# Performance work log

Measured on AMD Instinct MI355X. Metric: run time of the kernel, lower is better.

The kernel has to match this reference:

```python
import jax, jax.numpy as jnp
import numpy as np

N, F, B = 4096, 2048, 2048


def setup_inputs() -> dict:
    key = jax.random.key(0)
    ks = jax.random.split(key, 11)
    s_h = 1.0 / np.sqrt(F).astype(np.float32)
    s_x = 1.0 / np.sqrt(B).astype(np.float32)
    inp = {
        "behavior": jax.random.normal(ks[0], (N, B), jnp.float32),
        "h0": jax.random.normal(ks[1], (N, F), jnp.float32),
        "c0": jax.random.normal(ks[2], (N, F), jnp.float32),
        "Wi_h": jax.random.normal(ks[3], (F, F), jnp.float32) * s_h,
        "Wi_x": jax.random.normal(ks[4], (B, F), jnp.float32) * s_x,
        "bi": jnp.zeros((F,), jnp.float32),
        "Wf_h": jax.random.normal(ks[5], (F, F), jnp.float32) * s_h,
        "Wf_x": jax.random.normal(ks[6], (B, F), jnp.float32) * s_x,
        "bf": jnp.zeros((F,), jnp.float32),
        "Wg_h": jax.random.normal(ks[7], (F, F), jnp.float32) * s_h,
        "Wg_x": jax.random.normal(ks[8], (B, F), jnp.float32) * s_x,
        "bg": jnp.zeros((F,), jnp.float32),
        "Wo_h": jax.random.normal(ks[9], (F, F), jnp.float32) * s_h,
        "Wo_x": jax.random.normal(ks[10], (B, F), jnp.float32) * s_x,
        "bo": jnp.zeros((F,), jnp.float32),
    }
    return inp


def reference(behavior, h0, c0, Wi_h, Wi_x, bi, Wf_h, Wf_x, bf,
              Wg_h, Wg_x, bg, Wo_h, Wo_x, bo):
    # Single-step LSTM cell: each gate is a two-input linear proj (h, behavior)
    def proj(Wh, Wx, b):
        return h0 @ Wh + behavior @ Wx + b  # [N, F]

    i = jax.nn.sigmoid(proj(Wi_h, Wi_x, bi))
    f = jax.nn.sigmoid(proj(Wf_h, Wf_x, bf))
    g = jnp.tanh(proj(Wg_h, Wg_x, bg))
    o = jax.nn.sigmoid(proj(Wo_h, Wo_x, bo))
    c = f * c0 + i * g
    h = o * jnp.tanh(c)
    return h
```

## Files before the change

kernel.cpp:

```cpp
#include <hip/hip_runtime.h>
#include <stdint.h>

#define N_ROWS 4096
#define F_DIM  2048
#define B_DIM  2048
#define K_DIM  4096

typedef __attribute__((ext_vector_type(8)))  __bf16 bf16x8;
typedef __attribute__((ext_vector_type(16))) float  f32x16;
typedef unsigned short u16;

__device__ __forceinline__ u16 f2bf(float x) {
  unsigned int u = __float_as_uint(x);
  u += 0x7fffu + ((u >> 16) & 1u);
  return (u16)(u >> 16);
}

__device__ __forceinline__ void async_copy16(const void* g, void* l) {
  __builtin_amdgcn_global_load_lds(
      (const __attribute__((address_space(1))) void*)g,
      (__attribute__((address_space(3))) void*)l, 16, 0, 0);
}

__device__ __forceinline__ float sigmoid_f(float x) {
  return 1.0f / (1.0f + __expf(-x));
}
__device__ __forceinline__ float tanh_f(float x) {
  float e2 = __expf(2.0f * x);
  return 1.0f - 2.0f / (e2 + 1.0f);
}

__device__ __forceinline__ f32x16 mm(bf16x8 a, bf16x8 b, f32x16 c) {
  return __builtin_amdgcn_mfma_f32_32x32x16_bf16(a, b, c, 0, 0, 0);
}

__global__ __launch_bounds__(256) void pack_x_kernel(
    const float* __restrict__ h0, const float* __restrict__ behavior,
    u16* __restrict__ Xc)
{
  int tid = blockIdx.x * 256 + threadIdx.x;
  int row = tid >> 9;
  int k0  = (tid & 511) * 8;
  const float* src = (k0 < F_DIM) ? (h0 + (size_t)row * F_DIM + k0)
                                  : (behavior + (size_t)row * B_DIM + (k0 - F_DIM));
  const float4* s4 = (const float4*)src;
  float4 a = s4[0], b = s4[1];
  uint4 o;
  o.x = (unsigned)f2bf(a.x) | ((unsigned)f2bf(a.y) << 16);
  o.y = (unsigned)f2bf(a.z) | ((unsigned)f2bf(a.w) << 16);
  o.z = (unsigned)f2bf(b.x) | ((unsigned)f2bf(b.y) << 16);
  o.w = (unsigned)f2bf(b.z) | ((unsigned)f2bf(b.w) << 16);
  *(uint4*)(Xc + (size_t)tid * 8) = o;
}

__global__ __launch_bounds__(256) void pack_w_kernel(
    const float* __restrict__ wi_h, const float* __restrict__ wi_x,
    const float* __restrict__ wf_h, const float* __restrict__ wf_x,
    const float* __restrict__ wg_h, const float* __restrict__ wg_x,
    const float* __restrict__ wo_h, const float* __restrict__ wo_x,
    u16* __restrict__ WT)
{
  __shared__ float tileT[32 * 65];
  int g = blockIdx.z;
  const float* Wh = (g == 0) ? wi_h : (g == 1) ? wf_h : (g == 2) ? wg_h : wo_h;
  const float* Wx = (g == 0) ? wi_x : (g == 1) ? wf_x : (g == 2) ? wg_x : wo_x;
  int fb = blockIdx.x * 32;
  int kb = blockIdx.y * 64;
  const float* W = (kb < F_DIM) ? Wh : Wx;
  int kofs = (kb < F_DIM) ? kb : (kb - F_DIM);

  int t  = threadIdx.x;
  int c4 = t & 7;
  int kr = t >> 3;
#pragma unroll
  for (int p = 0; p < 2; ++p) {
    int k_l = kr + p * 32;
    float4 v = *(const float4*)(W + (size_t)(kofs + k_l) * F_DIM + fb + c4 * 4);
    tileT[(c4 * 4 + 0) * 65 + k_l] = v.x;
    tileT[(c4 * 4 + 1) * 65 + k_l] = v.y;
    tileT[(c4 * 4 + 2) * 65 + k_l] = v.z;
    tileT[(c4 * 4 + 3) * 65 + k_l] = v.w;
  }
  __syncthreads();
  {
    int f_l = t >> 3;
    int k8  = (t & 7) * 8;
    const float* s = tileT + f_l * 65 + k8;
    uint4 o;
    o.x = (unsigned)f2bf(s[0]) | ((unsigned)f2bf(s[1]) << 16);
    o.y = (unsigned)f2bf(s[2]) | ((unsigned)f2bf(s[3]) << 16);
    o.z = (unsigned)f2bf(s[4]) | ((unsigned)f2bf(s[5]) << 16);
    o.w = (unsigned)f2bf(s[6]) | ((unsigned)f2bf(s[7]) << 16);
    *(uint4*)(WT + ((size_t)g * F_DIM + fb + f_l) * K_DIM + kb + k8) = o;
  }
}

__global__ __launch_bounds__(512, 2) void lstm_gemm_kernel(
    const u16* __restrict__ Xc, const u16* __restrict__ WT,
    const float* __restrict__ c0,
    const float* __restrict__ bi, const float* __restrict__ bff,
    const float* __restrict__ bg, const float* __restrict__ bo,
    float* __restrict__ out)
{
  __shared__ u16 Ls[32768];

  const int tid  = threadIdx.x;
  const int lane = tid & 63;
  const int wv   = tid >> 6;
  const int bm   = blockIdx.x;
  const int bn   = blockIdx.y;

  const int rw   = wv & 3;
  const int fh   = wv >> 2;
  const int l31  = lane & 31;
  const int half = lane >> 5;
  const int swb  = (l31 >> 1) & 3;

  const u16* aSrc[2];
  const u16* bSrc[2];
#pragma unroll
  for (int p = 0; p < 2; ++p) {
    int c = p * 512 + tid;
    int r = c >> 2, s = c & 3;
    int o = s ^ ((r >> 1) & 3);
    aSrc[p] = Xc + (size_t)(bm * 256 + r) * K_DIM + o * 8;
    int g = c >> 8, cc = c & 255;
    int rb = cc >> 2, sb2 = cc & 3;
    int ob = sb2 ^ ((rb >> 1) & 3);
    bSrc[p] = WT + ((size_t)g * F_DIM + bn * 64 + rb) * K_DIM + ob * 8;
  }
  const unsigned ub = (unsigned)(tid & ~63) * 16u;

  f32x16 acc[4][2];
#pragma unroll
  for (int g = 0; g < 4; ++g)
#pragma unroll
    for (int rh = 0; rh < 2; ++rh)
#pragma unroll
      for (int r = 0; r < 16; ++r) acc[g][rh][r] = 0.f;

#pragma unroll
  for (int p = 0; p < 2; ++p) {
    async_copy16(aSrc[p], (char*)Ls + p * 8192 + ub);
    async_copy16(bSrc[p], (char*)Ls + 16384 + p * 8192 + ub);
  }
#pragma unroll
  for (int p = 0; p < 2; ++p) { aSrc[p] += 32; bSrc[p] += 32; }

  int cur = 0;
  for (int kt = 0; kt < 128; ++kt) {
    const int nb = cur ^ 1;
    char* LdsN = (char*)Ls + nb * 32768;
    const u16* Lb = Ls + cur * 16384;
    const u16* Ab0 = Lb + (rw * 64 +      l31) * 32;
    const u16* Ab1 = Lb + (rw * 64 + 32 + l31) * 32;
    const u16* Bb  = Lb + 8192 + (fh * 32 + l31) * 32;

    if (kt < 127) {
      async_copy16(aSrc[0], LdsN + ub);
      async_copy16(bSrc[0], LdsN + 16384 + ub);
      asm volatile("s_waitcnt vmcnt(2)" ::: "memory");
    } else {
      asm volatile("s_waitcnt vmcnt(0)" ::: "memory");
    }
    __builtin_amdgcn_s_barrier();
    {
      const int sw8 = (half ^ swb) * 8;
      bf16x8 af0 = *(const bf16x8*)(Ab0 + sw8);
      bf16x8 af1 = *(const bf16x8*)(Ab1 + sw8);
      bf16x8 bfr[4];
#pragma unroll
      for (int g = 0; g < 4; ++g)
        bfr[g] = *(const bf16x8*)(Bb + g * 2048 + sw8);
      __builtin_amdgcn_s_setprio(1);
#pragma unroll
      for (int g = 0; g < 4; ++g) {
        acc[g][0] = mm(af0, bfr[g], acc[g][0]);
        acc[g][1] = mm(af1, bfr[g], acc[g][1]);
      }
      __builtin_amdgcn_s_setprio(0);
    }
    __builtin_amdgcn_s_barrier();

    {
      const int sw8 = ((2 + half) ^ swb) * 8;
      bf16x8 af0 = *(const bf16x8*)(Ab0 + sw8);
      bf16x8 af1 = *(const bf16x8*)(Ab1 + sw8);
      bf16x8 bfr[4];
#pragma unroll
      for (int g = 0; g < 4; ++g)
        bfr[g] = *(const bf16x8*)(Bb + g * 2048 + sw8);
      if (kt < 127) {
        async_copy16(aSrc[1], LdsN + 8192 + ub);
        async_copy16(bSrc[1], LdsN + 16384 + 8192 + ub);
      }
      __builtin_amdgcn_s_barrier();
      __builtin_amdgcn_s_setprio(1);
#pragma unroll
      for (int g = 0; g < 4; ++g) {
        acc[g][0] = mm(af0, bfr[g], acc[g][0]);
        acc[g][1] = mm(af1, bfr[g], acc[g][1]);
      }
      __builtin_amdgcn_s_setprio(0);
    }
    asm volatile("s_waitcnt lgkmcnt(0)" ::: "memory");
    __builtin_amdgcn_s_barrier();

#pragma unroll
    for (int p = 0; p < 2; ++p) { aSrc[p] += 32; bSrc[p] += 32; }
    cur ^= 1;
  }

  {
    int f = bn * 64 + fh * 32 + l31;
    float b0 = bi[f], b1 = bff[f], b2 = bg[f], b3 = bo[f];
#pragma unroll
    for (int rh = 0; rh < 2; ++rh) {
      int row_base = bm * 256 + rw * 64 + rh * 32 + 4 * half;
#pragma unroll
      for (int r = 0; r < 16; ++r) {
        int row = row_base + (r & 3) + 8 * (r >> 2);
        size_t idx = (size_t)row * F_DIM + f;
        float pi = acc[0][rh][r] + b0;
        float pf = acc[1][rh][r] + b1;
        float pg = acc[2][rh][r] + b2;
        float po = acc[3][rh][r] + b3;
        float iv = sigmoid_f(pi);
        float fv = sigmoid_f(pf);
        float gv = tanh_f(pg);
        float ov = sigmoid_f(po);
        float cv = fv * c0[idx] + iv * gv;
        out[idx] = ov * tanh_f(cv);
      }
    }
  }
}

extern "C" void kernel_launch(void* const* d_in, const int* in_sizes, int n_in,
                              void* d_out, int out_size, void* d_ws, size_t ws_size,
                              hipStream_t stream) {
  const float* behavior = (const float*)d_in[0];
  const float* h0       = (const float*)d_in[1];
  const float* c0       = (const float*)d_in[2];
  const float* Wi_h     = (const float*)d_in[3];
  const float* Wi_x     = (const float*)d_in[4];
  const float* bi       = (const float*)d_in[5];
  const float* Wf_h     = (const float*)d_in[6];
  const float* Wf_x     = (const float*)d_in[7];
  const float* bf       = (const float*)d_in[8];
  const float* Wg_h     = (const float*)d_in[9];
  const float* Wg_x     = (const float*)d_in[10];
  const float* bg       = (const float*)d_in[11];
  const float* Wo_h     = (const float*)d_in[12];
  const float* Wo_x     = (const float*)d_in[13];
  const float* bo       = (const float*)d_in[14];
  float* out = (float*)d_out;

  u16* Xc = (u16*)d_ws;
  u16* WT = Xc + (size_t)N_ROWS * K_DIM;

  pack_x_kernel<<<dim3(N_ROWS * (K_DIM / 8) / 256), 256, 0, stream>>>(h0, behavior, Xc);
  pack_w_kernel<<<dim3(F_DIM / 32, K_DIM / 64, 4), 256, 0, stream>>>(
      Wi_h, Wi_x, Wf_h, Wf_x, Wg_h, Wg_x, Wo_h, Wo_x, WT);
  lstm_gemm_kernel<<<dim3(N_ROWS / 256, F_DIM / 64), 512, 0, stream>>>(
      Xc, WT, c0, bi, bf, bg, bo, out);
}
```

Baseline: 536.0 us.

## Double K tile to 64 per stage with 8-wide XOR swizzle and fewer barriers

Each pipeline stage now covers 64 K elements instead of 32, so the loop runs 64 iterations with 8 async copies per thread per stage. The intermediate barriers and split prefetch of the old two-half structure are gone. The LDS swizzle changes from a 4-way to an 8-way XOR pattern to match the 128-byte row stride. LDS use doubles to 128 KB per block, which may hurt occupancy under the two-blocks-per-CU launch bound and will exceed the per-block LDS limit if it is 64 KB.

```diff
diff --git a/kernel.cpp b/kernel.cpp
--- a/kernel.cpp
+++ b/kernel.cpp
@@ -102,7 +102,7 @@
     const float* __restrict__ bg, const float* __restrict__ bo,
     float* __restrict__ out)
 {
-  __shared__ u16 Ls[32768];
+  __shared__ u16 Ls[2 * 32768];
 
   const int tid  = threadIdx.x;
   const int lane = tid & 63;
@@ -114,20 +114,23 @@
   const int fh   = wv >> 2;
   const int l31  = lane & 31;
   const int half = lane >> 5;
-  const int swb  = (l31 >> 1) & 3;
-
-  const u16* aSrc[2];
-  const u16* bSrc[2];
-#pragma unroll
-  for (int p = 0; p < 2; ++p) {
+  const int sA   = l31 & 7;
+
+  const u16* src[8];
+#pragma unroll
+  for (int p = 0; p < 8; ++p) {
     int c = p * 512 + tid;
-    int r = c >> 2, s = c & 3;
-    int o = s ^ ((r >> 1) & 3);
-    aSrc[p] = Xc + (size_t)(bm * 256 + r) * K_DIM + o * 8;
-    int g = c >> 8, cc = c & 255;
-    int rb = cc >> 2, sb2 = cc & 3;
-    int ob = sb2 ^ ((rb >> 1) & 3);
-    bSrc[p] = WT + ((size_t)g * F_DIM + bn * 64 + rb) * K_DIM + ob * 8;
+    if (p < 4) {
+      int r = c >> 3, s = c & 7;
+      int o = s ^ (r & 7);
+      src[p] = Xc + (size_t)(bm * 256 + r) * K_DIM + o * 8;
+    } else {
+      int cb = c - 2048;
+      int g = cb >> 9, cc = cb & 511;
+      int rb = cc >> 3, sb = cc & 7;
+      int ob = sb ^ (rb & 7);
+      src[p] = WT + ((size_t)g * F_DIM + bn * 64 + rb) * K_DIM + ob * 8;
+    }
   }
   const unsigned ub = (unsigned)(tid & ~63) * 16u;
 
@@ -140,38 +143,39 @@
       for (int r = 0; r < 16; ++r) acc[g][rh][r] = 0.f;
 
 #pragma unroll
-  for (int p = 0; p < 2; ++p) {
-    async_copy16(aSrc[p], (char*)Ls + p * 8192 + ub);
-    async_copy16(bSrc[p], (char*)Ls + 16384 + p * 8192 + ub);
-  }
-#pragma unroll
-  for (int p = 0; p < 2; ++p) { aSrc[p] += 32; bSrc[p] += 32; }
+  for (int p = 0; p < 8; ++p)
+    async_copy16(src[p], (char*)Ls + p * 8192 + ub);
+#pragma unroll
+  for (int p = 0; p < 8; ++p) src[p] += 64;
 
   int cur = 0;
-  for (int kt = 0; kt < 128; ++kt) {
-    const int nb = cur ^ 1;
-    char* LdsN = (char*)Ls + nb * 32768;
-    const u16* Lb = Ls + cur * 16384;
-    const u16* Ab0 = Lb + (rw * 64 +      l31) * 32;
-    const u16* Ab1 = Lb + (rw * 64 + 32 + l31) * 32;
-    const u16* Bb  = Lb + 8192 + (fh * 32 + l31) * 32;
-
-    if (kt < 127) {
-      async_copy16(aSrc[0], LdsN + ub);
-      async_copy16(bSrc[0], LdsN + 16384 + ub);
-      asm volatile("s_waitcnt vmcnt(2)" ::: "memory");
+  for (int kt = 0; kt < 64; ++kt) {
+    char* LdsN = (char*)Ls + (cur ^ 1) * 65536;
+    const u16* Lb = Ls + cur * 32768;
+
+    if (kt < 63) {
+#pragma unroll
+      for (int p = 0; p < 8; ++p)
+        async_copy16(src[p], LdsN + p * 8192 + ub);
+      asm volatile("s_waitcnt vmcnt(8)" ::: "memory");
     } else {
       asm volatile("s_waitcnt vmcnt(0)" ::: "memory");
     }
     __builtin_amdgcn_s_barrier();
-    {
-      const int sw8 = (half ^ swb) * 8;
-      bf16x8 af0 = *(const bf16x8*)(Ab0 + sw8);
-      bf16x8 af1 = *(const bf16x8*)(Ab1 + sw8);
+
+    const u16* Arow0 = Lb + (rw * 64 +      l31) * 64;
+    const u16* Arow1 = Lb + (rw * 64 + 32 + l31) * 64;
+    const u16* Bbase = Lb + 16384 + (fh * 32 + l31) * 64;
+
+#pragma unroll
+    for (int c = 0; c < 4; ++c) {
+      const int sw8 = ((c * 2 + half) ^ sA) * 8;
+      bf16x8 af0 = *(const bf16x8*)(Arow0 + sw8);
+      bf16x8 af1 = *(const bf16x8*)(Arow1 + sw8);
       bf16x8 bfr[4];
 #pragma unroll
       for (int g = 0; g < 4; ++g)
-        bfr[g] = *(const bf16x8*)(Bb + g * 2048 + sw8);
+        bfr[g] = *(const bf16x8*)(Bbase + g * 4096 + sw8);
       __builtin_amdgcn_s_setprio(1);
 #pragma unroll
       for (int g = 0; g < 4; ++g) {
@@ -180,34 +184,12 @@
       }
       __builtin_amdgcn_s_setprio(0);
     }
-    __builtin_amdgcn_s_barrier();
-
-    {
-      const int sw8 = ((2 + half) ^ swb) * 8;
-      bf16x8 af0 = *(const bf16x8*)(Ab0 + sw8);
-      bf16x8 af1 = *(const bf16x8*)(Ab1 + sw8);
-      bf16x8 bfr[4];
-#pragma unroll
-      for (int g = 0; g < 4; ++g)
-        bfr[g] = *(const bf16x8*)(Bb + g * 2048 + sw8);
-      if (kt < 127) {
-        async_copy16(aSrc[1], LdsN + 8192 + ub);
-        async_copy16(bSrc[1], LdsN + 16384 + 8192 + ub);
-      }
-      __builtin_amdgcn_s_barrier();
-      __builtin_amdgcn_s_setprio(1);
-#pragma unroll
-      for (int g = 0; g < 4; ++g) {
-        acc[g][0] = mm(af0, bfr[g], acc[g][0]);
-        acc[g][1] = mm(af1, bfr[g], acc[g][1]);
-      }
-      __builtin_amdgcn_s_setprio(0);
-    }
+
     asm volatile("s_waitcnt lgkmcnt(0)" ::: "memory");
     __builtin_amdgcn_s_barrier();
 
 #pragma unroll
-    for (int p = 0; p < 2; ++p) { aSrc[p] += 32; bSrc[p] += 32; }
+    for (int p = 0; p < 8; ++p) src[p] += 64;
     cur ^= 1;
   }
 
```

New measurement: 511.4 us. 1.05x faster.
